# Kernel tuning notes

Measured on AMD Instinct MI355X. Metric: run time of the kernel, lower is better.

The kernel has to match this reference:

```python
import jax, jax.numpy as jnp
import numpy as np

B, NH, T, H, W = 2, 4, 8, 14, 14
DIM = 384
HD = DIM // NH  # 96 = head_dim = depthwise conv channels
N = T * H * W  # 1568 tokens, no cls
EPS = 1e-6


def _dwconv3d(x, w):
    # x: [BN, C, T, H, W], w: [C, 1, 3, 3, 3]; depthwise conv, stride 1, pad 1
    return jax.lax.conv_general_dilated(
        x, w, window_strides=(1, 1, 1), padding=[(1, 1)] * 3,
        feature_group_count=x.shape[1],
        dimension_numbers=('NCDHW', 'OIDHW', 'NCDHW'))


def _layernorm(x, g, b):
    m = jnp.mean(x, axis=-1, keepdims=True)
    v = jnp.var(x, axis=-1, keepdims=True)
    return (x - m) * jax.lax.rsqrt(v + EPS) * g + b


def _attention_pool(x4, conv_w, ln_g, ln_b, t, h, w):
    # x4: [B, nh, L, c] with L = t*h*w (no cls token)
    Bq, n, L, c = x4.shape
    y = x4.reshape(Bq * n, t, h, w, c).transpose(0, 4, 1, 2, 3)  # [(b nh), c, t, h, w]
    y = _dwconv3d(y, conv_w)
    y = y.transpose(0, 2, 3, 4, 1).reshape(Bq, n, L, c)
    return _layernorm(y, ln_g, ln_b)


def setup_inputs() -> dict:
    key = jax.random.key(0)
    ks = jax.random.split(key, 12)
    inp = {
        'x': jax.random.normal(ks[0], (B, N, DIM), jnp.float32),
        'qkv_w': jax.random.normal(ks[1], (3 * DIM, DIM), jnp.float32) * 0.02,
        'proj_w': jax.random.normal(ks[2], (DIM, DIM), jnp.float32) * 0.02,
        'proj_b': jnp.zeros((DIM,), jnp.float32),
        'pool_q_w': jax.random.normal(ks[3], (HD, 1, 3, 3, 3), jnp.float32) * 0.1,
        'pool_k_w': jax.random.normal(ks[4], (HD, 1, 3, 3, 3), jnp.float32) * 0.1,
        'pool_v_w': jax.random.normal(ks[5], (HD, 1, 3, 3, 3), jnp.float32) * 0.1,
        'norm_q_w': jnp.ones((HD,), jnp.float32), 'norm_q_b': jnp.zeros((HD,), jnp.float32),
        'norm_k_w': jnp.ones((HD,), jnp.float32), 'norm_k_b': jnp.zeros((HD,), jnp.float32),
        'norm_v_w': jnp.ones((HD,), jnp.float32), 'norm_v_b': jnp.zeros((HD,), jnp.float32),
        'rel_pos_h': jax.random.normal(ks[6], (2 * H - 1, HD), jnp.float32) * 0.02,
        'rel_pos_w': jax.random.normal(ks[7], (2 * W - 1, HD), jnp.float32) * 0.02,
        'rel_pos_t': jax.random.normal(ks[8], (2 * T - 1, HD), jnp.float32) * 0.02,
        't': T, 'h': H, 'w': W,
    }
    return inp


def reference(x, qkv_w, proj_w, proj_b, pool_q_w, pool_k_w, pool_v_w,
              norm_q_w, norm_q_b, norm_k_w, norm_k_b, norm_v_w, norm_v_b,
              rel_pos_h, rel_pos_w, rel_pos_t, t, h, w):
    Bq, Nq, _ = x.shape
    # fused QKV projection (qkv_bias=False)
    qkv = (x @ qkv_w.T).reshape(Bq, Nq, 3, NH, HD).transpose(2, 0, 3, 1, 4)
    q, k, v = qkv[0], qkv[1], qkv[2]  # [B, nh, N, hd]
    # pooled Q/K/V: depthwise conv3d + LayerNorm (stride 1 -> shapes preserved)
    q = _attention_pool(q, pool_q_w, norm_q_w, norm_q_b, t, h, w)
    k = _attention_pool(k, pool_k_w, norm_k_w, norm_k_b, t, h, w)
    v = _attention_pool(v, pool_v_w, norm_v_w, norm_v_b, t, h, w)

    scale = HD ** -0.5
    attn = jnp.einsum('bnqc,bnkc->bnqk', q * scale, k)  # [B, nh, N, N]

    # decomposed relative position biases (q_shape == k_shape, ratios == 1)
    dist_h = jnp.arange(h)[:, None] - jnp.arange(h)[None, :] + (h - 1)
    dist_w = jnp.arange(w)[:, None] - jnp.arange(w)[None, :] + (w - 1)
    dist_t = jnp.arange(t)[:, None] - jnp.arange(t)[None, :] + (t - 1)
    Rh = rel_pos_h[dist_h]  # [h, h, c]
    Rw = rel_pos_w[dist_w]  # [w, w, c]
    Rt = rel_pos_t[dist_t]  # [t, t, c]

    r_q = q.reshape(Bq, NH, t, h, w, HD)
    rel_h = jnp.einsum('bnthwc,hkc->bnthwk', r_q, Rh)  # [B,nh,t,h,w,kh]
    rel_w = jnp.einsum('bnthwc,wkc->bnthwk', r_q, Rw)  # [B,nh,t,h,w,kw]
    rel_t = jnp.einsum('bnthwc,tkc->bnthwk', r_q, Rt)  # [B,nh,t,h,w,kt]

    attn8 = attn.reshape(Bq, NH, t, h, w, t, h, w)
    attn8 = (attn8
             + rel_h[:, :, :, :, :, None, :, None]
             + rel_w[:, :, :, :, :, None, None, :]
             + rel_t[:, :, :, :, :, :, None, None])
    attn = jax.nn.softmax(attn8.reshape(Bq, NH, Nq, Nq), axis=-1)

    out = jnp.einsum('bnqk,bnkc->bnqc', attn, v)
    out = out + q  # residual pooling
    out = out.transpose(0, 2, 1, 3).reshape(Bq, Nq, DIM)
    out = out @ proj_w.T + proj_b
    return out
```

## Files before the change

kernel.cpp:

```cpp
#include <hip/hip_runtime.h>

#define B_    2
#define NH_   4
#define T_    8
#define H_    14
#define W_    14
#define HW_   196
#define HD_   96
#define DIM_  384
#define N_    1568
#define BH_   (B_*NH_)
#define BN_   (B_*N_)
#define BHN_  (BH_*N_)
#define CAUG_ 160

typedef unsigned short bf_t;
typedef unsigned int   u32;
typedef __attribute__((ext_vector_type(8))) short bf16x8;
typedef __attribute__((ext_vector_type(4))) float f32x4;

#define LOG2E 1.4426950408889634f
#define QSCALE_LOG2E 0.14724445f

static __device__ __forceinline__ float lo16(u32 v){ union{u32 i; float f;}x; x.i = v<<16;           return x.f; }
static __device__ __forceinline__ float hi16(u32 v){ union{u32 i; float f;}x; x.i = v & 0xffff0000u; return x.f; }
static __device__ __forceinline__ float b2f(bf_t v){ union{u32 i; float f;}x; x.i = ((u32)v)<<16;    return x.f; }
static __device__ __forceinline__ bf_t  f2b(float f){
  union{float f; u32 i;} x; x.f = f;
  return (bf_t)((x.i + 0x7fffu + ((x.i>>16)&1u)) >> 16);
}
static __device__ __forceinline__ u32 pack2(float a, float b){
  return (u32)f2b(a) | ((u32)f2b(b) << 16);
}
static __device__ __forceinline__ size_t ftidx(int row, int k){
  return ((((size_t)(row>>4))*12 + (k>>5))*64 + ((k>>3)&3)*16 + (row&15))*8 + (k&7);
}

#define NA_ (BN_*DIM_)
#define NB_ (3*DIM_*DIM_)
#define NC_ (DIM_*DIM_)
#define CAST_BLOCKS ((NA_+NB_+NC_)/4/256)

__global__ __launch_bounds__(256) void k_cast(
    const float* __restrict__ a, bf_t* __restrict__ ad,
    const float* __restrict__ b, bf_t* __restrict__ bd,
    const float* __restrict__ c, bf_t* __restrict__ cd,
    const float* __restrict__ wq, const float* __restrict__ wk,
    const float* __restrict__ wv, float* __restrict__ tq,
    float* __restrict__ tk, float* __restrict__ tv){
  if (blockIdx.x < CAST_BLOCKS){
    const int i = blockIdx.x*256 + threadIdx.x;
    const int i4 = i*4;
    float4 v; bf_t* dst; int row, k;
    if (i4 < NA_){
      v = ((const float4*)a)[i];
      dst = ad; row = i4/DIM_; k = i4%DIM_;
    } else if (i4 < NA_+NB_){
      const int f = i4 - NA_;
      v = ((const float4*)b)[i - NA_/4];
      dst = bd; row = f/DIM_; k = f%DIM_;
    } else {
      const int f = i4 - NA_ - NB_;
      v = ((const float4*)c)[i - (NA_+NB_)/4];
      dst = cd; row = f/DIM_; k = f%DIM_;
    }
    ushort4 o; o.x = f2b(v.x); o.y = f2b(v.y); o.z = f2b(v.z); o.w = f2b(v.w);
    *(ushort4*)(dst + ftidx(row, k)) = o;
  } else {
    const int idx = (blockIdx.x - CAST_BLOCKS)*256 + threadIdx.x;
    if (idx >= 3*HD_*27) return;
    const int t = idx / (HD_*27), rem = idx % (HD_*27);
    const int ch = rem / 27, j = rem % 27;
    const float* s = (t==0)? wq : (t==1)? wk : wv;
    float* d       = (t==0)? tq : (t==1)? tk : tv;
    d[j*HD_ + ch] = s[ch*27 + j];
  }
}

__global__ __launch_bounds__(256) void k_qkv(const bf_t* __restrict__ Xt,
    const bf_t* __restrict__ Wt,
    bf_t* __restrict__ q, bf_t* __restrict__ k, bf_t* __restrict__ v){
  const int wid = threadIdx.x >> 6, lane = threadIdx.x & 63;
  const int wr = wid & 1, wc = wid >> 1;
  const int nl = lane & 15, quad = lane >> 4;
  const int r0 = blockIdx.x*64 + wr*32;
  const int mt0 = r0 >> 4;
  const int nt0 = blockIdx.y*8 + wc*4;
  f32x4 acc[2][4];
  #pragma unroll
  for (int i = 0; i < 2; ++i)
    #pragma unroll
    for (int j = 0; j < 4; ++j) acc[i][j] = (f32x4){0.f,0.f,0.f,0.f};
  const bf_t* A0 = Xt + ((size_t)mt0*12*64 + lane)*8;
  const bf_t* B0 = Wt + ((size_t)nt0*12*64 + lane)*8;
  #pragma unroll 2
  for (int k0 = 0; k0 < 12; ++k0){
    const bf16x8 a0 = *(const bf16x8*)(A0 + k0*512);
    const bf16x8 a1 = *(const bf16x8*)(A0 + 12*512 + k0*512);
    bf16x8 bf[4];
    #pragma unroll
    for (int j = 0; j < 4; ++j) bf[j] = *(const bf16x8*)(B0 + (size_t)(j*12 + k0)*512);
    #pragma unroll
    for (int j = 0; j < 4; ++j){
      acc[0][j] = __builtin_amdgcn_mfma_f32_16x16x32_bf16(a0, bf[j], acc[0][j], 0, 0, 0);
      acc[1][j] = __builtin_amdgcn_mfma_f32_16x16x32_bf16(a1, bf[j], acc[1][j], 0, 0, 0);
    }
  }
  #pragma unroll
  for (int i = 0; i < 2; ++i){
    #pragma unroll
    for (int r = 0; r < 4; ++r){
      const int m  = r0 + i*16 + quad*4 + r;
      const int bb = m / N_, nn = m % N_;
      #pragma unroll
      for (int j = 0; j < 4; ++j){
        const int col = (nt0 + j)*16 + nl;
        const int s = col / DIM_, rem = col - s*DIM_;
        const int head = rem / HD_, hc = rem % HD_;
        bf_t* dst = (s==0) ? q : (s==1) ? k : v;
        dst[((size_t)(bb*NH_ + head)*N_ + nn)*HD_ + hc] = f2b(acc[i][j][r]);
      }
    }
  }
}

static __device__ __forceinline__ void ln_butterfly(
    float v0, float v1, float& mean, float& rstd){
  float s  = v0 + v1;
  float s2 = v0*v0 + v1*v1;
  #pragma unroll
  for (int off = 32; off > 0; off >>= 1){
    s  += __shfl_xor(s,  off);
    s2 += __shfl_xor(s2, off);
  }
  mean = s * (1.f/HD_);
  const float var = fmaxf(s2*(1.f/HD_) - mean*mean, 0.f);
  rstd = rsqrtf(var + 1e-6f);
}

union PoolSM {
  bf_t  slab[162][HD_];
  float qtmp[4][4][HD_];
  u32   vres[16][48];
};

__global__ __launch_bounds__(256) void k_pool_slab(
    const bf_t* __restrict__ qr_, const bf_t* __restrict__ kr_, const bf_t* __restrict__ vr_,
    const float* __restrict__ wtq, const float* __restrict__ wtk, const float* __restrict__ wtv,
    const float* __restrict__ gq, const float* __restrict__ bq,
    const float* __restrict__ gk, const float* __restrict__ bk,
    const float* __restrict__ gv, const float* __restrict__ bv,
    const float* __restrict__ rph, const float* __restrict__ rpw,
    const float* __restrict__ rpt,
    bf_t* __restrict__ qp, bf_t* __restrict__ Qaug,
    bf_t* __restrict__ Kt, bf_t* __restrict__ Vtt){
  __shared__ __align__(16) PoolSM sm;
  const int wid = threadIdx.x >> 6, lane = threadIdx.x & 63;
  const int bh   = blockIdx.x & 7;
  const int rest = blockIdx.x >> 3;
  const int sec  = rest / 98;
  const int tok0 = (rest % 98)*16;
  const bf_t*  src = (sec==0)? qr_ : (sec==1)? kr_ : vr_;
  const float* wt  = (sec==0)? wtq : (sec==1)? wtk : wtv;
  const float* g   = (sec==0)? gq  : (sec==1)? gk  : gv;
  const float* be  = (sec==0)? bq  : (sec==1)? bk  : bv;
  const bf_t* base = src + (size_t)bh*N_*HD_;

  const int c0 = (lane < 48) ? 2*lane : 0;
  float2 wcur[3], wnxt[3];
  #pragma unroll
  for (int dw = 0; dw < 3; ++dw) wcur[dw] = *(const float2*)(wt + dw*HD_ + c0);
  const float gg0 = g[c0], gg1 = g[c0+1], be0 = be[c0], be1 = be[c0+1];

  {
    uint4 stg[8];
    #pragma unroll
    for (int it = 0; it < 8; ++it){
      const int li = threadIdx.x + it*256;
      const int lc = (li < 162*12) ? li : (162*12 - 1);
      const int rw = lc / 12, ss = lc % 12;
      const int aa = rw/54, bb2 = (rw%54)/18, cc = rw%18;
      int nn = tok0 + (aa-1)*HW_ + (bb2-1)*W_ + (cc-1);
      nn = min(max(nn, 0), N_-1);
      stg[it] = *(const uint4*)(base + (size_t)nn*HD_ + ss*8);
    }
    #pragma unroll
    for (int it = 0; it < 8; ++it){
      const int li = threadIdx.x + it*256;
      if (li < 162*12){
        const int rw = li / 12, ss = li % 12;
        *(uint4*)&sm.slab[rw][ss*8] = stg[it];
      }
    }
  }
  __syncthreads();

  int tt[4], hh[4], ww[4];
  u32 mr[4];
  #pragma unroll
  for (int tk = 0; tk < 4; ++tk){
    const int n = tok0 + wid*4 + tk;
    tt[tk] = n / HW_;
    const int rm = n % HW_;
    hh[tk] = rm / W_; ww[tk] = rm % W_;
    const u32 wb = (ww[tk] > 0 ? 1u : 0u) | 2u | (ww[tk] < W_-1 ? 4u : 0u);
    const u32 h9 = (hh[tk] > 0 ? wb : 0u) | (wb << 3) | (hh[tk] < H_-1 ? (wb << 6) : 0u);
    mr[tk] = (tt[tk] > 0 ? h9 : 0u) | (h9 << 9) | (tt[tk] < T_-1 ? (h9 << 18) : 0u);
  }

  float v0[4] = {0.f,0.f,0.f,0.f}, v1[4] = {0.f,0.f,0.f,0.f};
  u32 rr[6], rrn[6];
  #pragma unroll
  for (int s = 0; s < 6; ++s) rr[s] = *(const u32*)&sm.slab[wid*4 + s][c0];
  #pragma unroll 1
  for (int j9 = 0; j9 < 9; ++j9){
    if (j9 < 8){
      const int jn = j9 + 1;
      const int rbn = (jn/3)*54 + (jn%3)*18 + wid*4;
      #pragma unroll
      for (int s = 0; s < 6; ++s) rrn[s] = *(const u32*)&sm.slab[rbn + s][c0];
      #pragma unroll
      for (int dw = 0; dw < 3; ++dw)
        wnxt[dw] = *(const float2*)(wt + (jn*3 + dw)*HD_ + c0);
    }
    #pragma unroll
    for (int tk = 0; tk < 4; ++tk){
      #pragma unroll
      for (int dw = 0; dw < 3; ++dw){
        const u32 d = (mr[tk] & (1u << dw)) ? rr[tk+dw] : 0u;
        v0[tk] = fmaf(wcur[dw].x, lo16(d), v0[tk]);
        v1[tk] = fmaf(wcur[dw].y, hi16(d), v1[tk]);
      }
      mr[tk] >>= 3;
    }
    #pragma unroll
    for (int s = 0; s < 6; ++s) rr[s] = rrn[s];
    #pragma unroll
    for (int dw = 0; dw < 3; ++dw) wcur[dw] = wnxt[dw];
  }
  #pragma unroll
  for (int tk = 0; tk < 4; ++tk){
    float a = v0[tk], b = v1[tk];
    if (lane >= 48){ a = 0.f; b = 0.f; }
    float mean, rstd;
    ln_butterfly(a, b, mean, rstd);
    v0[tk] = (a - mean)*rstd*gg0 + be0;
    v1[tk] = (b - mean)*rstd*gg1 + be1;
  }

  if (sec == 0){
    __syncthreads();
    #pragma unroll
    for (int tk = 0; tk < 4; ++tk){
      const int n = tok0 + wid*4 + tk;
      const int token = bh*N_ + n;
      if (lane < 48){
        ((u32*)qp)  [(size_t)token*48 + lane] = pack2(v0[tk], v1[tk]);
        ((u32*)Qaug)[(size_t)token*80 + lane] = pack2(v0[tk]*QSCALE_LOG2E, v1[tk]*QSCALE_LOG2E);
        *(float2*)&sm.qtmp[wid][tk][c0] = make_float2(v0[tk], v1[tk]);
      }
    }
    #pragma unroll
    for (int tk = 0; tk < 4; ++tk){
      const int n = tok0 + wid*4 + tk;
      const int token = bh*N_ + n;
      if (lane < 36){
        const float* tb; int idx;
        if (lane < 14)      { tb = rph; idx = hh[tk] - lane      + 13; }
        else if (lane < 28) { tb = rpw; idx = ww[tk] - (lane-14) + 13; }
        else                { tb = rpt; idx = tt[tk] - (lane-28) +  7; }
        const float4* t4 = (const float4*)(tb + (size_t)idx*HD_);
        const float4* q4 = (const float4*)&sm.qtmp[wid][tk][0];
        float ap[4] = {0.f, 0.f, 0.f, 0.f};
        #pragma unroll
        for (int i = 0; i < 24; ++i){
          const float4 rv = t4[i];
          const float4 qv = q4[i];
          ap[i & 3] = fmaf(qv.x, rv.x,
                      fmaf(qv.y, rv.y,
                      fmaf(qv.z, rv.z,
                      fmaf(qv.w, rv.w, ap[i & 3]))));
        }
        const float acc = (ap[0] + ap[1]) + (ap[2] + ap[3]);
        Qaug[(size_t)token*CAUG_ + HD_ + lane] = f2b(acc * LOG2E);
      } else {
        Qaug[(size_t)token*CAUG_ + HD_ + lane] = 0;
      }
    }
  } else if (sec == 1){
    #pragma unroll
    for (int tk = 0; tk < 4; ++tk){
      const int n = tok0 + wid*4 + tk;
      const int tl = n >> 4, nr = n & 15;
      if (lane < 48){
        const size_t idx = ((((size_t)bh*98 + tl)*5 + (lane>>4))*64
                           + ((lane&15)>>2)*16 + nr)*4 + (lane&3);
        ((u32*)Kt)[idx] = pack2(v0[tk], v1[tk]);
      } else {
        const int m = lane - 48;
        u32 pr_[2];
        #pragma unroll
        for (int h2 = 0; h2 < 2; ++h2){
          u32 w_ = 0;
          #pragma unroll
          for (int e = 0; e < 2; ++e){
            const int jj = 4*m + 2*h2 + e;
            bool on = (jj < 14) ? (jj == hh[tk]) : (jj < 28) ? (jj-14 == ww[tk])
                     : (jj < 36) ? (jj-28 == tt[tk]) : false;
            if (on) w_ |= (0x3F80u << (16*e));
          }
          pr_[h2] = w_;
        }
        const size_t bidx = ((((size_t)bh*98 + tl)*5 + (3 + (m>>3)))*64
                            + ((m&7)>>1)*16 + nr)*4 + 2*(m&1);
        *(uint2*)((u32*)Kt + bidx) = make_uint2(pr_[0], pr_[1]);
      }
    }
  } else {
    __syncthreads();
    #pragma unroll
    for (int tk = 0; tk < 4; ++tk){
      if (lane < 48) sm.vres[wid*4 + tk][lane] = pack2(v0[tk], v1[tk]);
    }
    __syncthreads();
    if (threadIdx.x < 2*HD_){
      const int grp = threadIdx.x / HD_, c = threadIdx.x % HD_;
      const int t0g = grp*8;
      u32 o[4];
      #pragma unroll
      for (int i = 0; i < 4; ++i){
        const u32 a = sm.vres[t0g + 2*i][c>>1], b = sm.vres[t0g + 2*i+1][c>>1];
        const u32 ra = (c&1) ? (a >> 16) : (a & 0xffffu);
        const u32 rb = (c&1) ? (b >> 16) : (b & 0xffffu);
        o[i] = ra | (rb << 16);
      }
      const int n0g = tok0 + t0g;
      const int pr = n0g >> 5, qd = (n0g & 31) >> 3;
      bf_t* dst = Vtt + ((((size_t)bh*49 + pr)*6 + (c>>4))*64 + qd*16 + (c&15))*8;
      *(uint4*)dst = make_uint4(o[0], o[1], o[2], o[3]);
    }
  }
}

__global__ __launch_bounds__(512) void k_attn(
    const bf_t* __restrict__ Qaug, const bf_t* __restrict__ Kt,
    const bf_t* __restrict__ Vtt, const bf_t* __restrict__ qp,
    bf_t* __restrict__ attb){
  __shared__ __align__(16) short Pb[8][16][40];
  __shared__ bf_t Os[8][16][96];
  __shared__ float ms[8][16], ls[8][16];
  const int wid = threadIdx.x >> 6, lane = threadIdx.x & 63;
  const int bh = blockIdx.x & 7, qt = blockIdx.x >> 3;
  const int q0 = qt*16;
  const int nl = lane & 15, quad = lane >> 4;

  bf16x8 qa[5];
  {
    const bf_t* Qrow = Qaug + ((size_t)bh*N_ + q0 + nl)*CAUG_ + quad*8;
    #pragma unroll
    for (int i = 0; i < 5; ++i) qa[i] = *(const bf16x8*)(Qrow + i*32);
  }
  short* Pw = &Pb[wid][0][0];

  f32x4 O[6];
  #pragma unroll
  for (int i = 0; i < 6; ++i) O[i] = (f32x4){0.f,0.f,0.f,0.f};
  float mc[4]   = {0.f,0.f,0.f,0.f};
  float rmax[4] = {-3e38f,-3e38f,-3e38f,-3e38f};
  float l[4]    = {0.f,0.f,0.f,0.f};

  auto s_tile = [&](int tl, int half){
    const bf_t* Kp = Kt + (((size_t)bh*98 + tl)*5*64 + lane)*8;
    f32x4 s = (f32x4){0.f,0.f,0.f,0.f};
    #pragma unroll
    for (int i = 0; i < 5; ++i)
      s = __builtin_amdgcn_mfma_f32_16x16x32_bf16(qa[i], *(const bf16x8*)(Kp + i*512), s, 0, 0, 0);
    #pragma unroll
    for (int r = 0; r < 4; ++r){
      rmax[r] = fmaxf(rmax[r], s[r]);
      const float p = exp2f(s[r] - mc[r]);
      l[r] += p;
      Pw[(quad*4 + r)*40 + half*16 + nl] = (short)f2b(p);
    }
  };
  auto rescale = [&](){
    #pragma unroll
    for (int r = 0; r < 4; ++r){
      float tm = rmax[r];
      tm = fmaxf(tm, __shfl_xor(tm, 1));
      tm = fmaxf(tm, __shfl_xor(tm, 2));
      tm = fmaxf(tm, __shfl_xor(tm, 4));
      tm = fmaxf(tm, __shfl_xor(tm, 8));
      const float mn = fmaxf(mc[r], tm);
      const float al = exp2f(mc[r] - mn);
      mc[r] = mn; l[r] *= al;
      #pragma unroll
      for (int ct = 0; ct < 6; ++ct) O[ct][r] *= al;
    }
  };

  const int p0 = (wid == 0) ? 0 : (7 + 6*(wid-1));
  const int npairs = (wid == 0) ? 7 : 6;
  #pragma unroll 1
  for (int pi = 0; pi < npairs; ++pi){
    const int kp = p0 + pi;
    s_tile(2*kp,     0);
    s_tile(2*kp + 1, 1);
    const bf16x8 pa = *(const bf16x8*)(Pw + nl*40 + quad*8);
    const bf_t* Vp = Vtt + (((size_t)bh*49 + kp)*6*64 + lane)*8;
    #pragma unroll
    for (int ct = 0; ct < 6; ++ct)
      O[ct] = __builtin_amdgcn_mfma_f32_16x16x32_bf16(pa, *(const bf16x8*)(Vp + ct*512), O[ct], 0, 0, 0);
    if (pi == npairs-1) rescale();
  }

  #pragma unroll
  for (int r = 0; r < 4; ++r){
    float ls_ = l[r];
    ls_ += __shfl_xor(ls_, 1); ls_ += __shfl_xor(ls_, 2);
    ls_ += __shfl_xor(ls_, 4); ls_ += __shfl_xor(ls_, 8);
    if (nl == 0){ ms[wid][quad*4 + r] = mc[r]; ls[wid][quad*4 + r] = ls_; }
    #pragma unroll
    for (int ct = 0; ct < 6; ++ct) Os[wid][quad*4 + r][ct*16 + nl] = f2b(O[ct][r]);
  }
  __syncthreads();

  const int bb = bh >> 2, head = bh & 3;
  const int grow0 = bb*N_ + q0;
  for (int e = threadIdx.x; e < 16*96; e += 512){
    const int row = e / 96, col = e % 96;
    float mx = -3e38f;
    #pragma unroll
    for (int w = 0; w < 8; ++w) mx = fmaxf(mx, ms[w][row]);
    float L = 0.f, A = 0.f;
    #pragma unroll
    for (int w = 0; w < 8; ++w){
      const float wt = exp2f(ms[w][row] - mx);
      L += wt*ls[w][row];
      A += wt*b2f(Os[w][row][col]);
    }
    const float val = A/L + b2f(qp[((size_t)bh*N_ + q0 + row)*HD_ + col]);
    attb[ftidx(grow0 + row, head*HD_ + col)] = f2b(val);
  }
}

__global__ __launch_bounds__(256) void k_proj(const bf_t* __restrict__ At,
    const bf_t* __restrict__ Wpt, const float* __restrict__ pb,
    float* __restrict__ out){
  const int wid = threadIdx.x >> 6, lane = threadIdx.x & 63;
  const int wr = wid & 1, wc = wid >> 1;
  const int nl = lane & 15, quad = lane >> 4;
  const int r0 = blockIdx.x*64 + wr*32;
  const int mt0 = r0 >> 4;
  const int nt0 = blockIdx.y*8 + wc*4;
  f32x4 acc[2][4];
  #pragma unroll
  for (int i = 0; i < 2; ++i)
    #pragma unroll
    for (int j = 0; j < 4; ++j) acc[i][j] = (f32x4){0.f,0.f,0.f,0.f};
  const bf_t* A0 = At  + ((size_t)mt0*12*64 + lane)*8;
  const bf_t* B0 = Wpt + ((size_t)nt0*12*64 + lane)*8;
  #pragma unroll 2
  for (int k0 = 0; k0 < 12; ++k0){
    const bf16x8 a0 = *(const bf16x8*)(A0 + k0*512);
    const bf16x8 a1 = *(const bf16x8*)(A0 + 12*512 + k0*512);
    bf16x8 bf[4];
    #pragma unroll
    for (int j = 0; j < 4; ++j) bf[j] = *(const bf16x8*)(B0 + (size_t)(j*12 + k0)*512);
    #pragma unroll
    for (int j = 0; j < 4; ++j){
      acc[0][j] = __builtin_amdgcn_mfma_f32_16x16x32_bf16(a0, bf[j], acc[0][j], 0, 0, 0);
      acc[1][j] = __builtin_amdgcn_mfma_f32_16x16x32_bf16(a1, bf[j], acc[1][j], 0, 0, 0);
    }
  }
  #pragma unroll
  for (int i = 0; i < 2; ++i){
    #pragma unroll
    for (int r = 0; r < 4; ++r){
      const int m = r0 + i*16 + quad*4 + r;
      #pragma unroll
      for (int j = 0; j < 4; ++j){
        const int col = (nt0 + j)*16 + nl;
        out[(size_t)m*DIM_ + col] = acc[i][j][r] + pb[col];
      }
    }
  }
}

extern "C" void kernel_launch(void* const* d_in, const int* in_sizes, int n_in,
                              void* d_out, int out_size, void* d_ws, size_t ws_size,
                              hipStream_t stream){
  const float* x      = (const float*)d_in[0];
  const float* qkv_w  = (const float*)d_in[1];
  const float* proj_w = (const float*)d_in[2];
  const float* proj_b = (const float*)d_in[3];
  const float* pqw    = (const float*)d_in[4];
  const float* pkw    = (const float*)d_in[5];
  const float* pvw    = (const float*)d_in[6];
  const float* nqw    = (const float*)d_in[7];
  const float* nqb    = (const float*)d_in[8];
  const float* nkw    = (const float*)d_in[9];
  const float* nkb    = (const float*)d_in[10];
  const float* nvw    = (const float*)d_in[11];
  const float* nvb    = (const float*)d_in[12];
  const float* rph    = (const float*)d_in[13];
  const float* rpw    = (const float*)d_in[14];
  const float* rpt    = (const float*)d_in[15];

  char* p = (char*)d_ws;
  const size_t RAW = (size_t)BH_*N_*HD_*2;
  const size_t AUG = (size_t)BH_*N_*CAUG_*2;
  bf_t* xb     = (bf_t*)(p);
  bf_t* wqkvb  = (bf_t*)(p + RAW);
  bf_t* wprojb = (bf_t*)(p + RAW + 884736);
  char* p2 = p + RAW + 884736 + 294912;
  bf_t* raw_q  = (bf_t*)(p2);
  bf_t* raw_k  = (bf_t*)(p2 + RAW);
  bf_t* raw_v  = (bf_t*)(p2 + 2*RAW);
  bf_t* attb   = raw_q;
  bf_t* qp     = (bf_t*)(p2 + 3*RAW);
  bf_t* Qaug   = (bf_t*)(p2 + 4*RAW);
  bf_t* Kt     = (bf_t*)(p2 + 4*RAW + AUG);
  bf_t* Vtt    = (bf_t*)(p2 + 4*RAW + 2*AUG);
  float* wtq   = (float*)(p2 + 4*RAW + 2*AUG + RAW);
  float* wtk   = wtq + 27*HD_;
  float* wtv   = wtk + 27*HD_;

  k_cast     <<<CAST_BLOCKS + 31, 256, 0, stream>>>(x, xb, qkv_w, wqkvb, proj_w, wprojb,
                                                    pqw, pkw, pvw, wtq, wtk, wtv);
  k_qkv      <<<dim3(BN_/64, 9),  256, 0, stream>>>(xb, wqkvb, raw_q, raw_k, raw_v);
  k_pool_slab<<<3*784,            256, 0, stream>>>(raw_q, raw_k, raw_v,
                                                    wtq, wtk, wtv,
                                                    nqw, nqb, nkw, nkb, nvw, nvb,
                                                    rph, rpw, rpt,
                                                    qp, Qaug, Kt, Vtt);
  k_attn     <<<BH_*98,           512, 0, stream>>>(Qaug, Kt, Vtt, qp, attb);
  k_proj     <<<dim3(BN_/64, 3),  256, 0, stream>>>(attb, wprojb, proj_b, (float*)d_out);
}
```

Measured before the change: 193.4 us.

## Process two query tiles per wave in attention to reuse K/V fragments

Each attention block now handles 32 query rows with 4 waves instead of 16 rows with 8 waves, so each wave runs two independent 16-row MFMA streams that share every K and V fragment load. This halves global K/V traffic per query and doubles the independent MFMA work per wave. The running max is no longer subtracted inside the loop: exponentials are computed unshifted, and the final rescale clamps the max at zero. That relies on scores staying small enough not to overflow. The block count halves and per-wave register pressure roughly doubles, which may lower occupancy.

```diff
diff --git a/kernel.cpp b/kernel.cpp
--- a/kernel.cpp
+++ b/kernel.cpp
@@ -342,99 +342,133 @@
   }
 }
 
-__global__ __launch_bounds__(512) void k_attn(
+__global__ __launch_bounds__(256) void k_attn(
     const bf_t* __restrict__ Qaug, const bf_t* __restrict__ Kt,
     const bf_t* __restrict__ Vtt, const bf_t* __restrict__ qp,
     bf_t* __restrict__ attb){
-  __shared__ __align__(16) short Pb[8][16][40];
-  __shared__ bf_t Os[8][16][96];
-  __shared__ float ms[8][16], ls[8][16];
+  __shared__ __align__(16) short Pb[4][16][80];
+  __shared__ bf_t Os[4][32][96];
+  __shared__ float ms[4][32], ls[4][32];
   const int wid = threadIdx.x >> 6, lane = threadIdx.x & 63;
   const int bh = blockIdx.x & 7, qt = blockIdx.x >> 3;
-  const int q0 = qt*16;
+  const int q0 = qt*32;
   const int nl = lane & 15, quad = lane >> 4;
 
-  bf16x8 qa[5];
+  bf16x8 qaA[5], qaB[5];
   {
-    const bf_t* Qrow = Qaug + ((size_t)bh*N_ + q0 + nl)*CAUG_ + quad*8;
-    #pragma unroll
-    for (int i = 0; i < 5; ++i) qa[i] = *(const bf16x8*)(Qrow + i*32);
+    const bf_t* QrowA = Qaug + ((size_t)bh*N_ + q0 + nl)*CAUG_ + quad*8;
+    const bf_t* QrowB = QrowA + (size_t)16*CAUG_;
+    #pragma unroll
+    for (int i = 0; i < 5; ++i){
+      qaA[i] = *(const bf16x8*)(QrowA + i*32);
+      qaB[i] = *(const bf16x8*)(QrowB + i*32);
+    }
   }
   short* Pw = &Pb[wid][0][0];
 
-  f32x4 O[6];
-  #pragma unroll
-  for (int i = 0; i < 6; ++i) O[i] = (f32x4){0.f,0.f,0.f,0.f};
-  float mc[4]   = {0.f,0.f,0.f,0.f};
-  float rmax[4] = {-3e38f,-3e38f,-3e38f,-3e38f};
-  float l[4]    = {0.f,0.f,0.f,0.f};
+  f32x4 OA[6], OB[6];
+  #pragma unroll
+  for (int i = 0; i < 6; ++i){ OA[i] = (f32x4){0.f,0.f,0.f,0.f}; OB[i] = (f32x4){0.f,0.f,0.f,0.f}; }
+  float rmaxA[4] = {-3e38f,-3e38f,-3e38f,-3e38f}, lA[4] = {0.f,0.f,0.f,0.f}, mcA[4];
+  float rmaxB[4] = {-3e38f,-3e38f,-3e38f,-3e38f}, lB[4] = {0.f,0.f,0.f,0.f}, mcB[4];
 
   auto s_tile = [&](int tl, int half){
     const bf_t* Kp = Kt + (((size_t)bh*98 + tl)*5*64 + lane)*8;
-    f32x4 s = (f32x4){0.f,0.f,0.f,0.f};
-    #pragma unroll
-    for (int i = 0; i < 5; ++i)
-      s = __builtin_amdgcn_mfma_f32_16x16x32_bf16(qa[i], *(const bf16x8*)(Kp + i*512), s, 0, 0, 0);
+    f32x4 sA = (f32x4){0.f,0.f,0.f,0.f};
+    f32x4 sB = (f32x4){0.f,0.f,0.f,0.f};
+    #pragma unroll
+    for (int i = 0; i < 5; ++i){
+      const bf16x8 kf = *(const bf16x8*)(Kp + i*512);
+      sA = __builtin_amdgcn_mfma_f32_16x16x32_bf16(qaA[i], kf, sA, 0, 0, 0);
+      sB = __builtin_amdgcn_mfma_f32_16x16x32_bf16(qaB[i], kf, sB, 0, 0, 0);
+    }
     #pragma unroll
     for (int r = 0; r < 4; ++r){
-      rmax[r] = fmaxf(rmax[r], s[r]);
-      const float p = exp2f(s[r] - mc[r]);
-      l[r] += p;
-      Pw[(quad*4 + r)*40 + half*16 + nl] = (short)f2b(p);
+      rmaxA[r] = fmaxf(rmaxA[r], sA[r]);
+      const float pA_ = exp2f(sA[r]);
+      lA[r] += pA_;
+      Pw[(quad*4 + r)*80 + half*16 + nl] = (short)f2b(pA_);
+      rmaxB[r] = fmaxf(rmaxB[r], sB[r]);
+      const float pB_ = exp2f(sB[r]);
+      lB[r] += pB_;
+      Pw[(quad*4 + r)*80 + 40 + half*16 + nl] = (short)f2b(pB_);
     }
   };
   auto rescale = [&](){
     #pragma unroll
     for (int r = 0; r < 4; ++r){
-      float tm = rmax[r];
+      float tm = rmaxA[r];
       tm = fmaxf(tm, __shfl_xor(tm, 1));
       tm = fmaxf(tm, __shfl_xor(tm, 2));
       tm = fmaxf(tm, __shfl_xor(tm, 4));
       tm = fmaxf(tm, __shfl_xor(tm, 8));
-      const float mn = fmaxf(mc[r], tm);
-      const float al = exp2f(mc[r] - mn);
-      mc[r] = mn; l[r] *= al;
-      #pragma unroll
-      for (int ct = 0; ct < 6; ++ct) O[ct][r] *= al;
+      const float mn = fmaxf(0.f, tm);
+      const float al = exp2f(-mn);
+      mcA[r] = mn; lA[r] *= al;
+      #pragma unroll
+      for (int ct = 0; ct < 6; ++ct) OA[ct][r] *= al;
+      float tb = rmaxB[r];
+      tb = fmaxf(tb, __shfl_xor(tb, 1));
+      tb = fmaxf(tb, __shfl_xor(tb, 2));
+      tb = fmaxf(tb, __shfl_xor(tb, 4));
+      tb = fmaxf(tb, __shfl_xor(tb, 8));
+      const float mnb = fmaxf(0.f, tb);
+      const float alb = exp2f(-mnb);
+      mcB[r] = mnb; lB[r] *= alb;
+      #pragma unroll
+      for (int ct = 0; ct < 6; ++ct) OB[ct][r] *= alb;
     }
   };
 
-  const int p0 = (wid == 0) ? 0 : (7 + 6*(wid-1));
-  const int npairs = (wid == 0) ? 7 : 6;
+  const int p0 = (wid == 0) ? 0 : (13 + 12*(wid-1));
+  const int npairs = (wid == 0) ? 13 : 12;
   #pragma unroll 1
   for (int pi = 0; pi < npairs; ++pi){
     const int kp = p0 + pi;
     s_tile(2*kp,     0);
     s_tile(2*kp + 1, 1);
-    const bf16x8 pa = *(const bf16x8*)(Pw + nl*40 + quad*8);
+    const bf16x8 paA = *(const bf16x8*)(Pw + nl*80 + quad*8);
+    const bf16x8 paB = *(const bf16x8*)(Pw + nl*80 + 40 + quad*8);
     const bf_t* Vp = Vtt + (((size_t)bh*49 + kp)*6*64 + lane)*8;
     #pragma unroll
-    for (int ct = 0; ct < 6; ++ct)
-      O[ct] = __builtin_amdgcn_mfma_f32_16x16x32_bf16(pa, *(const bf16x8*)(Vp + ct*512), O[ct], 0, 0, 0);
+    for (int ct = 0; ct < 6; ++ct){
+      const bf16x8 vf = *(const bf16x8*)(Vp + ct*512);
+      OA[ct] = __builtin_amdgcn_mfma_f32_16x16x32_bf16(paA, vf, OA[ct], 0, 0, 0);
+      OB[ct] = __builtin_amdgcn_mfma_f32_16x16x32_bf16(paB, vf, OB[ct], 0, 0, 0);
+    }
     if (pi == npairs-1) rescale();
   }
 
   #pragma unroll
   for (int r = 0; r < 4; ++r){
-    float ls_ = l[r];
-    ls_ += __shfl_xor(ls_, 1); ls_ += __shfl_xor(ls_, 2);
-    ls_ += __shfl_xor(ls_, 4); ls_ += __shfl_xor(ls_, 8);
-    if (nl == 0){ ms[wid][quad*4 + r] = mc[r]; ls[wid][quad*4 + r] = ls_; }
-    #pragma unroll
-    for (int ct = 0; ct < 6; ++ct) Os[wid][quad*4 + r][ct*16 + nl] = f2b(O[ct][r]);
+    float la_ = lA[r];
+    la_ += __shfl_xor(la_, 1); la_ += __shfl_xor(la_, 2);
+    la_ += __shfl_xor(la_, 4); la_ += __shfl_xor(la_, 8);
+    float lb_ = lB[r];
+    lb_ += __shfl_xor(lb_, 1); lb_ += __shfl_xor(lb_, 2);
+    lb_ += __shfl_xor(lb_, 4); lb_ += __shfl_xor(lb_, 8);
+    if (nl == 0){
+      ms[wid][quad*4 + r]      = mcA[r]; ls[wid][quad*4 + r]      = la_;
+      ms[wid][16 + quad*4 + r] = mcB[r]; ls[wid][16 + quad*4 + r] = lb_;
+    }
+    #pragma unroll
+    for (int ct = 0; ct < 6; ++ct){
+      Os[wid][quad*4 + r][ct*16 + nl]      = f2b(OA[ct][r]);
+      Os[wid][16 + quad*4 + r][ct*16 + nl] = f2b(OB[ct][r]);
+    }
   }
   __syncthreads();
 
   const int bb = bh >> 2, head = bh & 3;
   const int grow0 = bb*N_ + q0;
-  for (int e = threadIdx.x; e < 16*96; e += 512){
+  for (int e = threadIdx.x; e < 32*96; e += 256){
     const int row = e / 96, col = e % 96;
     float mx = -3e38f;
     #pragma unroll
-    for (int w = 0; w < 8; ++w) mx = fmaxf(mx, ms[w][row]);
+    for (int w = 0; w < 4; ++w) mx = fmaxf(mx, ms[w][row]);
     float L = 0.f, A = 0.f;
     #pragma unroll
-    for (int w = 0; w < 8; ++w){
+    for (int w = 0; w < 4; ++w){
       const float wt = exp2f(ms[w][row] - mx);
       L += wt*ls[w][row];
       A += wt*b2f(Os[w][row][col]);
@@ -534,6 +568,6 @@
                                                     nqw, nqb, nkw, nkb, nvw, nvb,
                                                     rph, rpw, rpt,
                                                     qp, Qaug, Kt, Vtt);
-  k_attn     <<<BH_*98,           512, 0, stream>>>(Qaug, Kt, Vtt, qp, attb);
+  k_attn     <<<BH_*49,           256, 0, stream>>>(Qaug, Kt, Vtt, qp, attb);
   k_proj     <<<dim3(BN_/64, 3),  256, 0, stream>>>(attb, wprojb, proj_b, (float*)d_out);
 }
```

Measured after the change: 195.3 us. About the same (+1.0%).
